# Kernel optimization log

Hardware: AMD Instinct MI355X
Metric: run time of the kernel (lower is better)

The kernel has to match this reference:

```python
import jax, jax.numpy as jnp
import numpy as np

N = 8192
HID = 64
TAU = 0.8
LAMBDA = 0.5
POS_DENSITY = 0.005


def setup_inputs() -> dict:
    key = jax.random.key(0)
    k1, k2, k3, k4, k5, k6, k7 = jax.random.split(key, 7)
    x1 = jax.random.normal(k1, (N, HID), dtype=jnp.float32)
    x2 = jax.random.normal(k2, (N, HID), dtype=jnp.float32)
    # xavier_uniform with gain=1.414 for square [HID, HID] linears
    limit = 1.414 * np.sqrt(6.0 / (HID + HID))
    W1 = jax.random.uniform(k3, (HID, HID), dtype=jnp.float32, minval=-limit, maxval=limit)
    b1 = jnp.zeros((HID,), dtype=jnp.float32)
    W2 = jax.random.uniform(k4, (HID, HID), dtype=jnp.float32, minval=-limit, maxval=limit)
    b2 = jnp.zeros((HID,), dtype=jnp.float32)
    pm = (jax.random.uniform(k5, (N, N), dtype=jnp.float32) < POS_DENSITY).astype(jnp.float32)
    positive_matrix = jnp.maximum(pm, jnp.eye(N, dtype=jnp.float32))
    return {"x1": x1, "x2": x2, "W1": W1, "b1": b1, "W2": W2, "b2": b2,
            "positive_matrix": positive_matrix}


def _project(x, W1, b1, W2, b2):
    # nn.Linear(hidden, hidden) -> ELU -> nn.Linear(hidden, hidden)
    h = jax.nn.elu(x @ W1.T + b1)
    return h @ W2.T + b2


def _l2norm(z, eps=1e-12):
    # F.normalize(p=2, dim=1): x / max(||x||, eps)
    n = jnp.linalg.norm(z, axis=-1, keepdims=True)
    return z / jnp.maximum(n, eps)


def _sim(z1, z2, tau):
    return jnp.exp((_l2norm(z1) @ _l2norm(z2).T) / tau)  # [N, N]


def _masked_loss(sim_mat, pos):
    row = sim_mat / (jnp.sum(sim_mat, axis=-1, keepdims=True) + 1e-8)
    return -jnp.log(jnp.sum(row * pos, axis=-1) + 1e-8).mean()


def reference(x1, x2, W1, b1, W2, b2, positive_matrix):
    z1 = _project(x1, W1, b1, W2, b2)
    z2 = _project(x2, W1, b1, W2, b2)
    sc_mp = _sim(z1, z2, TAU)
    mp_sc = _sim(z2, z1, TAU)
    sc_loss = _masked_loss(sc_mp, positive_matrix)
    mp_loss = _masked_loss(mp_sc, positive_matrix)
    return sc_loss * LAMBDA + mp_loss * (1.0 - LAMBDA)
```

## Files before the change

### kernel.cpp

```cpp
#include <hip/hip_runtime.h>
#include <hip/hip_bf16.h>

#define N 8192
#define HID 64
#define JC 8

typedef __attribute__((ext_vector_type(4))) float f32x4;
typedef __attribute__((ext_vector_type(8))) __bf16 bf16x8;

__global__ __launch_bounds__(256) void proj_kernel(
    const float* __restrict__ x1, const float* __restrict__ x2,
    const float* __restrict__ W1, const float* __restrict__ b1,
    const float* __restrict__ W2, const float* __restrict__ b2,
    __bf16* __restrict__ Z1h, __bf16* __restrict__ Z2h)
{
  __shared__ __align__(16) float w1s[64*68];
  __shared__ __align__(16) float w2s[64*68];
  __shared__ __align__(16) float xs[4][64];
  __shared__ __align__(16) float hs[4][64];

  const int tid  = threadIdx.x;
  const int lane = tid & 63;
  const int w    = tid >> 6;

  for (int idx = tid; idx < 64*64; idx += 256) {
    int j = idx >> 6, k = idx & 63;
    w1s[j*68+k] = W1[idx];
    w2s[j*68+k] = W2[idx];
  }
  __syncthreads();

  const float bias1 = b1[lane];
  const float bias2 = b2[lane];

  const int wave_global = blockIdx.x * 4 + w;
  #pragma unroll 1
  for (int it = 0; it < 16; ++it) {
    int R = wave_global * 16 + it;
    const float* src; __bf16* dst;
    if (R < N) { src = x1 + (size_t)R*HID;      dst = Z1h + (size_t)R*HID; }
    else       { src = x2 + (size_t)(R-N)*HID;  dst = Z2h + (size_t)(R-N)*HID; }

    float xv = src[lane];
    xs[w][lane] = xv;
    float acc = bias1;
    #pragma unroll
    for (int qq = 0; qq < 16; ++qq) {
      f32x4 xq = *(const f32x4*)&xs[w][qq*4];
      f32x4 wq = *(const f32x4*)&w1s[lane*68 + qq*4];
      acc += xq.x*wq.x + xq.y*wq.y + xq.z*wq.z + xq.w*wq.w;
    }
    float h = acc > 0.f ? acc : expm1f(acc);
    hs[w][lane] = h;
    float acc2 = bias2;
    #pragma unroll
    for (int qq = 0; qq < 16; ++qq) {
      f32x4 hq = *(const f32x4*)&hs[w][qq*4];
      f32x4 wq = *(const f32x4*)&w2s[lane*68 + qq*4];
      acc2 += hq.x*wq.x + hq.y*wq.y + hq.z*wq.z + hq.w*wq.w;
    }
    float z = acc2;
    float ss = z*z;
    #pragma unroll
    for (int m = 1; m < 64; m <<= 1) ss += __shfl_xor(ss, m);
    float inv = 1.0f / fmaxf(sqrtf(ss), 1e-12f);
    dst[lane] = (__bf16)(z * inv);
  }
}

__global__ __launch_bounds__(256) void sim_kernel(
    const __bf16* __restrict__ Z1h, const __bf16* __restrict__ Z2h,
    const float* __restrict__ pos,
    float* __restrict__ rowsum1, float* __restrict__ num1,
    float* __restrict__ rowsum2, float* __restrict__ num2)
{
  const int tid  = threadIdx.x;
  const int lane = tid & 63;
  const int w    = tid >> 6;
  const int r16  = lane & 15;
  const int q    = lane >> 4;

  const int bi = blockIdx.x / JC;
  const int jc = blockIdx.x % JC;
  const int i0 = bi*64 + w*16;

  const __bf16* z1r = Z1h + (size_t)(i0 + r16)*HID + q*8;
  const __bf16* z2r = Z2h + (size_t)(i0 + r16)*HID + q*8;
  bf16x8 a1lo = *(const bf16x8*)(z1r);
  bf16x8 a1hi = *(const bf16x8*)(z1r + 32);
  bf16x8 a2lo = *(const bf16x8*)(z2r);
  bf16x8 a2hi = *(const bf16x8*)(z2r + 32);

  float s1[4] = {0.f,0.f,0.f,0.f}, n1[4] = {0.f,0.f,0.f,0.f};
  float s2[4] = {0.f,0.f,0.f,0.f}, n2[4] = {0.f,0.f,0.f,0.f};

  const int jbeg = jc * (N/JC);
  const int jend = jbeg + (N/JC);
  const float Cexp = 1.8033688011112042f;

  const float* pbase = pos + (size_t)(i0 + q*4)*N + r16;

  for (int j0 = jbeg; j0 < jend; j0 += 16) {
    const __bf16* zb2 = Z2h + (size_t)(j0 + r16)*HID + q*8;
    const __bf16* zb1 = Z1h + (size_t)(j0 + r16)*HID + q*8;
    bf16x8 b2lo = *(const bf16x8*)(zb2);
    bf16x8 b2hi = *(const bf16x8*)(zb2 + 32);
    bf16x8 b1lo = *(const bf16x8*)(zb1);
    bf16x8 b1hi = *(const bf16x8*)(zb1 + 32);

    const float* pp = pbase + j0;
    float p0 = pp[0];
    float p1 = pp[(size_t)N];
    float p2 = pp[(size_t)2*N];
    float p3 = pp[(size_t)3*N];

    f32x4 zero4 = {0.f,0.f,0.f,0.f};
    f32x4 d1 = __builtin_amdgcn_mfma_f32_16x16x32_bf16(a1lo, b2lo, zero4, 0,0,0);
    d1       = __builtin_amdgcn_mfma_f32_16x16x32_bf16(a1hi, b2hi, d1,    0,0,0);
    f32x4 d2 = __builtin_amdgcn_mfma_f32_16x16x32_bf16(a2lo, b1lo, zero4, 0,0,0);
    d2       = __builtin_amdgcn_mfma_f32_16x16x32_bf16(a2hi, b1hi, d2,    0,0,0);

    float pv[4] = {p0, p1, p2, p3};
    #pragma unroll
    for (int r = 0; r < 4; ++r) {
      float e1 = exp2f(d1[r] * Cexp);
      float e2 = exp2f(d2[r] * Cexp);
      s1[r] += e1; n1[r] += e1 * pv[r];
      s2[r] += e2; n2[r] += e2 * pv[r];
    }
  }

  #pragma unroll
  for (int r = 0; r < 4; ++r) {
    #pragma unroll
    for (int m = 1; m < 16; m <<= 1) {
      s1[r] += __shfl_xor(s1[r], m);
      n1[r] += __shfl_xor(n1[r], m);
      s2[r] += __shfl_xor(s2[r], m);
      n2[r] += __shfl_xor(n2[r], m);
    }
  }
  if (r16 == 0) {
    #pragma unroll
    for (int r = 0; r < 4; ++r) {
      int row = i0 + q*4 + r;
      atomicAdd(&rowsum1[row], s1[r]);
      atomicAdd(&num1[row],    n1[r]);
      atomicAdd(&rowsum2[row], s2[r]);
      atomicAdd(&num2[row],    n2[r]);
    }
  }
}

__global__ __launch_bounds__(256) void loss_kernel(
    const float* __restrict__ rowsum1, const float* __restrict__ num1,
    const float* __restrict__ rowsum2, const float* __restrict__ num2,
    float* __restrict__ out)
{
  __shared__ float part[4];
  const int tid = threadIdx.x, lane = tid & 63, w = tid >> 6;
  float acc = 0.f;
  for (int i = tid; i < N; i += 256) {
    float sc = -logf(num1[i]/(rowsum1[i]+1e-8f) + 1e-8f);
    float mp = -logf(num2[i]/(rowsum2[i]+1e-8f) + 1e-8f);
    acc += 0.5f*sc + 0.5f*mp;
  }
  #pragma unroll
  for (int m = 1; m < 64; m <<= 1) acc += __shfl_xor(acc, m);
  if (lane == 0) part[w] = acc;
  __syncthreads();
  if (tid == 0) out[0] = (part[0]+part[1]+part[2]+part[3]) * (1.0f/N);
}

extern "C" void kernel_launch(void* const* d_in, const int* in_sizes, int n_in,
                              void* d_out, int out_size, void* d_ws, size_t ws_size,
                              hipStream_t stream) {
  const float* x1  = (const float*)d_in[0];
  const float* x2  = (const float*)d_in[1];
  const float* W1  = (const float*)d_in[2];
  const float* b1  = (const float*)d_in[3];
  const float* W2  = (const float*)d_in[4];
  const float* b2  = (const float*)d_in[5];
  const float* pos = (const float*)d_in[6];

  char* ws = (char*)d_ws;
  __bf16* Z1h = (__bf16*)ws;
  __bf16* Z2h = (__bf16*)(ws + (size_t)N*HID*sizeof(__bf16));
  size_t zbytes = (size_t)2*N*HID*sizeof(__bf16);
  float* rowsum1 = (float*)(ws + zbytes);
  float* num1    = rowsum1 + N;
  float* rowsum2 = num1 + N;
  float* num2    = rowsum2 + N;

  hipMemsetAsync(ws + zbytes, 0, (size_t)4*N*sizeof(float), stream);
  proj_kernel<<<256, 256, 0, stream>>>(x1, x2, W1, b1, W2, b2, Z1h, Z2h);
  sim_kernel<<<128*JC, 256, 0, stream>>>(Z1h, Z2h, pos, rowsum1, num1, rowsum2, num2);
  loss_kernel<<<1, 256, 0, stream>>>(rowsum1, num1, rowsum2, num2, (float*)d_out);
}
```

Baseline: 491.0 us.

## Widen grids for projection, sim and loss kernels and unroll sim loop by two

Splits the similarity column range into 16 chunks instead of 8 and raises the projection grid from 256 to 1024 blocks, so each wave handles fewer rows. Widens the loss reduction to 1024 threads. The sim inner loop now loads two 16-column tiles of Z and the positive mask before computing, to expose more memory-level parallelism, and asks for an occupancy hint of 6 blocks. The trade-off is more atomics on the row sums and higher register pressure from the double-buffered loads.

Result: faster. 449.6 us (-8.4%).

```diff
diff --git a/kernel.cpp b/kernel.cpp
--- a/kernel.cpp
+++ b/kernel.cpp
@@ -3,7 +3,7 @@
 
 #define N 8192
 #define HID 64
-#define JC 8
+#define JC 16
 
 typedef __attribute__((ext_vector_type(4))) float f32x4;
 typedef __attribute__((ext_vector_type(8))) __bf16 bf16x8;
@@ -35,8 +35,8 @@
 
   const int wave_global = blockIdx.x * 4 + w;
   #pragma unroll 1
-  for (int it = 0; it < 16; ++it) {
-    int R = wave_global * 16 + it;
+  for (int it = 0; it < 4; ++it) {
+    int R = wave_global * 4 + it;
     const float* src; __bf16* dst;
     if (R < N) { src = x1 + (size_t)R*HID;      dst = Z1h + (size_t)R*HID; }
     else       { src = x2 + (size_t)(R-N)*HID;  dst = Z2h + (size_t)(R-N)*HID; }
@@ -68,7 +68,7 @@
   }
 }
 
-__global__ __launch_bounds__(256) void sim_kernel(
+__global__ __launch_bounds__(256, 6) void sim_kernel(
     const __bf16* __restrict__ Z1h, const __bf16* __restrict__ Z2h,
     const float* __restrict__ pos,
     float* __restrict__ rowsum1, float* __restrict__ num1,
@@ -100,33 +100,38 @@
 
   const float* pbase = pos + (size_t)(i0 + q*4)*N + r16;
 
-  for (int j0 = jbeg; j0 < jend; j0 += 16) {
-    const __bf16* zb2 = Z2h + (size_t)(j0 + r16)*HID + q*8;
-    const __bf16* zb1 = Z1h + (size_t)(j0 + r16)*HID + q*8;
-    bf16x8 b2lo = *(const bf16x8*)(zb2);
-    bf16x8 b2hi = *(const bf16x8*)(zb2 + 32);
-    bf16x8 b1lo = *(const bf16x8*)(zb1);
-    bf16x8 b1hi = *(const bf16x8*)(zb1 + 32);
-
-    const float* pp = pbase + j0;
-    float p0 = pp[0];
-    float p1 = pp[(size_t)N];
-    float p2 = pp[(size_t)2*N];
-    float p3 = pp[(size_t)3*N];
-
-    f32x4 zero4 = {0.f,0.f,0.f,0.f};
-    f32x4 d1 = __builtin_amdgcn_mfma_f32_16x16x32_bf16(a1lo, b2lo, zero4, 0,0,0);
-    d1       = __builtin_amdgcn_mfma_f32_16x16x32_bf16(a1hi, b2hi, d1,    0,0,0);
-    f32x4 d2 = __builtin_amdgcn_mfma_f32_16x16x32_bf16(a2lo, b1lo, zero4, 0,0,0);
-    d2       = __builtin_amdgcn_mfma_f32_16x16x32_bf16(a2hi, b1hi, d2,    0,0,0);
-
-    float pv[4] = {p0, p1, p2, p3};
-    #pragma unroll
-    for (int r = 0; r < 4; ++r) {
-      float e1 = exp2f(d1[r] * Cexp);
-      float e2 = exp2f(d2[r] * Cexp);
-      s1[r] += e1; n1[r] += e1 * pv[r];
-      s2[r] += e2; n2[r] += e2 * pv[r];
+  #pragma unroll 1
+  for (int j0 = jbeg; j0 < jend; j0 += 32) {
+    bf16x8 b2l[2], b2h[2], b1l[2], b1h[2];
+    float pv[2][4];
+    #pragma unroll
+    for (int c = 0; c < 2; ++c) {
+      const __bf16* zb2 = Z2h + (size_t)(j0 + c*16 + r16)*HID + q*8;
+      const __bf16* zb1 = Z1h + (size_t)(j0 + c*16 + r16)*HID + q*8;
+      b2l[c] = *(const bf16x8*)(zb2);
+      b2h[c] = *(const bf16x8*)(zb2 + 32);
+      b1l[c] = *(const bf16x8*)(zb1);
+      b1h[c] = *(const bf16x8*)(zb1 + 32);
+      const float* pp = pbase + j0 + c*16;
+      pv[c][0] = pp[0];
+      pv[c][1] = pp[(size_t)N];
+      pv[c][2] = pp[(size_t)2*N];
+      pv[c][3] = pp[(size_t)3*N];
+    }
+    #pragma unroll
+    for (int c = 0; c < 2; ++c) {
+      f32x4 zero4 = {0.f,0.f,0.f,0.f};
+      f32x4 d1 = __builtin_amdgcn_mfma_f32_16x16x32_bf16(a1lo, b2l[c], zero4, 0,0,0);
+      d1       = __builtin_amdgcn_mfma_f32_16x16x32_bf16(a1hi, b2h[c], d1,    0,0,0);
+      f32x4 d2 = __builtin_amdgcn_mfma_f32_16x16x32_bf16(a2lo, b1l[c], zero4, 0,0,0);
+      d2       = __builtin_amdgcn_mfma_f32_16x16x32_bf16(a2hi, b1h[c], d2,    0,0,0);
+      #pragma unroll
+      for (int r = 0; r < 4; ++r) {
+        float e1 = exp2f(d1[r] * Cexp);
+        float e2 = exp2f(d2[r] * Cexp);
+        s1[r] += e1; n1[r] += e1 * pv[c][r];
+        s2[r] += e2; n2[r] += e2 * pv[c][r];
+      }
     }
   }
 
@@ -152,15 +157,15 @@
   }
 }
 
-__global__ __launch_bounds__(256) void loss_kernel(
+__global__ __launch_bounds__(1024) void loss_kernel(
     const float* __restrict__ rowsum1, const float* __restrict__ num1,
     const float* __restrict__ rowsum2, const float* __restrict__ num2,
     float* __restrict__ out)
 {
-  __shared__ float part[4];
+  __shared__ float part[16];
   const int tid = threadIdx.x, lane = tid & 63, w = tid >> 6;
   float acc = 0.f;
-  for (int i = tid; i < N; i += 256) {
+  for (int i = tid; i < N; i += 1024) {
     float sc = -logf(num1[i]/(rowsum1[i]+1e-8f) + 1e-8f);
     float mp = -logf(num2[i]/(rowsum2[i]+1e-8f) + 1e-8f);
     acc += 0.5f*sc + 0.5f*mp;
@@ -169,7 +174,12 @@
   for (int m = 1; m < 64; m <<= 1) acc += __shfl_xor(acc, m);
   if (lane == 0) part[w] = acc;
   __syncthreads();
-  if (tid == 0) out[0] = (part[0]+part[1]+part[2]+part[3]) * (1.0f/N);
+  if (tid == 0) {
+    float t = 0.f;
+    #pragma unroll
+    for (int k = 0; k < 16; ++k) t += part[k];
+    out[0] = t * (1.0f/N);
+  }
 }
 
 extern "C" void kernel_launch(void* const* d_in, const int* in_sizes, int n_in,
@@ -193,7 +203,7 @@
   float* num2    = rowsum2 + N;
 
   hipMemsetAsync(ws + zbytes, 0, (size_t)4*N*sizeof(float), stream);
-  proj_kernel<<<256, 256, 0, stream>>>(x1, x2, W1, b1, W2, b2, Z1h, Z2h);
+  proj_kernel<<<1024, 256, 0, stream>>>(x1, x2, W1, b1, W2, b2, Z1h, Z2h);
   sim_kernel<<<128*JC, 256, 0, stream>>>(Z1h, Z2h, pos, rowsum1, num1, rowsum2, num2);
-  loss_kernel<<<1, 256, 0, stream>>>(rowsum1, num1, rowsum2, num2, (float*)d_out);
-}
+  loss_kernel<<<1, 1024, 0, stream>>>(rowsum1, num1, rowsum2, num2, (float*)d_out);
+}
```
